# Kernel optimization log

Hardware: AMD Instinct MI355X
Metric: run time of the kernel (lower is better)

The kernel has to match this reference:

```python
import jax, jax.numpy as jnp
import numpy as np

B, N, E, NREG, DIN, F = 16, 20000, 640000, 2000, 128, 32
NEG_SLOPE = 0.2  # PyG GATConv default negative_slope


def setup_inputs() -> dict:
    key = jax.random.key(0)
    ks = jax.random.split(key, 10)
    x = jax.random.normal(ks[0], (B, N, DIN), dtype=jnp.float32)
    edge_src = jnp.sort(jax.random.randint(ks[1], (E,), 0, NREG, dtype=jnp.int64))
    edge_dst = jax.random.randint(ks[2], (E,), 0, N, dtype=jnp.int64)
    edge_attr = jax.random.uniform(ks[3], (B, E, 1), dtype=jnp.float32)
    # GATConv parameters (heads=1, concat=False, edge_dim=1)
    W = jax.random.normal(ks[4], (DIN, F), dtype=jnp.float32) * 0.05   # lin (shared src/dst)
    att_src = jax.random.normal(ks[5], (F,), dtype=jnp.float32) * 0.1
    att_dst = jax.random.normal(ks[6], (F,), dtype=jnp.float32) * 0.1
    lin_edge = jax.random.normal(ks[7], (1, F), dtype=jnp.float32) * 0.1
    att_edge = jax.random.normal(ks[8], (F,), dtype=jnp.float32) * 0.1
    bias = jax.random.normal(ks[9], (F,), dtype=jnp.float32) * 0.01
    return {"x": x, "edge_attr": edge_attr, "W": W, "att_src": att_src,
            "att_dst": att_dst, "lin_edge": lin_edge, "att_edge": att_edge,
            "bias": bias, "edge_src": edge_src, "edge_dst": edge_dst}


def _gat_regulon(x, eattr, W, att_src, att_dst, lin_edge, att_edge, bias,
                 src, dst):
    # x: [N, DIN], eattr: [E, 1]; src/dst: [E] int (src < NREG, sorted)
    h = x @ W                                  # [N, F]
    a_src = h @ att_src                        # [N]
    a_dst = h @ att_dst                        # [N]
    # add_self_loops=True with fill_value='mean' for edge_attr
    loop_attr = jnp.broadcast_to(jnp.mean(eattr, axis=0, keepdims=True), (N, 1))
    eattr_full = jnp.concatenate([eattr, loop_attr], axis=0)         # [E+N, 1]
    sl = jnp.arange(N, dtype=src.dtype)
    src_f = jnp.concatenate([src, sl])                               # [E+N]
    dst_f = jnp.concatenate([dst, sl])                               # [E+N]
    a_edge = (eattr_full @ lin_edge) @ att_edge                      # [E+N]
    alpha = jax.nn.leaky_relu(a_src[src_f] + a_dst[dst_f] + a_edge, NEG_SLOPE)
    # segment softmax over destination nodes (self-loops => no empty segment)
    m = jax.ops.segment_max(alpha, dst_f, num_segments=N)
    ex = jnp.exp(alpha - m[dst_f])
    s = jax.ops.segment_sum(ex, dst_f, num_segments=N)
    coef = ex / s[dst_f]                                             # [E+N]
    rep = jax.ops.segment_sum(coef[:, None] * h[src_f], dst_f, num_segments=N)
    rep = rep + bias                                                 # [N, F]
    # fused regulon pooling: out[i] = rep[i] + sum_{(i->t) in E} rep[t]
    pooled = jax.ops.segment_sum(rep[dst], src, num_segments=NREG)   # [NREG, F]
    return rep[:NREG] + pooled


def reference(x, edge_attr, W, att_src, att_dst, lin_edge, att_edge, bias,
              edge_src, edge_dst):
    fn = jax.vmap(lambda xi, ei: _gat_regulon(xi, ei, W, att_src, att_dst,
                                              lin_edge, att_edge, bias,
                                              edge_src, edge_dst))
    return fn(x, edge_attr)                                          # [B, NREG, F]
```

## Files before the change

### kernel.cpp

```cpp
#include <hip/hip_runtime.h>
#include <math.h>

#define B    16
#define N    20000
#define E    640000
#define NREG 2000
#define DIN  128
#define F    32
#define NEG  0.2f
#define BF   (B * F)
#define NCHUNK 8
#define CS   2500

typedef unsigned int uint;

__device__ inline uint bf16pair(float a, float b) {
    uint ua = __float_as_uint(a); ua = (ua + 0x7fffu + ((ua >> 16) & 1u)) >> 16;
    uint ub = __float_as_uint(b); ub = (ub + 0x7fffu + ((ub >> 16) & 1u)) >> 16;
    return ua | (ub << 16);
}
__device__ inline float bf16lo(uint v) { return __uint_as_float(v << 16); }
__device__ inline float bf16hi(uint v) { return __uint_as_float(v & 0xffff0000u); }

__global__ void k_hist(const int* __restrict__ dst, int* __restrict__ counts) {
    int e = blockIdx.x * blockDim.x + threadIdx.x;
    int stride = gridDim.x * blockDim.x;
    for (; e < E; e += stride)
        atomicAdd(&counts[dst[e]], 1);
}

__global__ void k_roff(const int* __restrict__ esrc, int* __restrict__ roff) {
    int r = blockIdx.x * blockDim.x + threadIdx.x;
    if (r > NREG) return;
    int lo = 0, hi = E;
    while (lo < hi) {
        int mid = (lo + hi) >> 1;
        if (esrc[mid] < r) lo = mid + 1; else hi = mid;
    }
    roff[r] = lo;
}

__global__ void k_scan(const int* __restrict__ in, int* __restrict__ out, int n) {
    __shared__ int sh[1024];
    int t = threadIdx.x;
    int chunk = (n + 1023) / 1024;
    int lo = t * chunk;
    int hi = lo + chunk; if (hi > n) hi = n;
    int local = 0;
    for (int i = lo; i < hi; ++i) local += in[i];
    sh[t] = local;
    __syncthreads();
    for (int d = 1; d < 1024; d <<= 1) {
        int v = (t >= d) ? sh[t - d] : 0;
        __syncthreads();
        sh[t] += v;
        __syncthreads();
    }
    int run = (t == 0) ? 0 : sh[t - 1];
    for (int i = lo; i < hi; ++i) { out[i] = run; run += in[i]; }
    if (t == 1023) out[n] = sh[1023];
}

__global__ void k_scatter(const int* __restrict__ src, const int* __restrict__ dst,
                          const int* __restrict__ off, int* __restrict__ cursor,
                          int* __restrict__ csr_src, int* __restrict__ pos_of_e) {
    int e = blockIdx.x * blockDim.x + threadIdx.x;
    int stride = gridDim.x * blockDim.x;
    for (; e < E; e += stride) {
        int d = dst[e];
        int pos = off[d] + atomicAdd(&cursor[d], 1);
        csr_src[pos] = src[e];
        pos_of_e[e] = pos;
    }
}

__global__ __launch_bounds__(256) void k_bucket(const int* __restrict__ edst,
                                                const int* __restrict__ roff,
                                                int* __restrict__ boff,
                                                int* __restrict__ pe_dst) {
    __shared__ int cnt[NCHUNK], pref[NCHUNK], cur[NCHUNK];
    int r = blockIdx.x;
    int t = threadIdx.x;
    int lo = roff[r], hi = roff[r + 1];
    if (t < NCHUNK) { cnt[t] = 0; cur[t] = 0; }
    __syncthreads();
    for (int e = lo + t; e < hi; e += 256)
        atomicAdd(&cnt[edst[e] / CS], 1);
    __syncthreads();
    if (t == 0) {
        int run = 0;
        #pragma unroll
        for (int c = 0; c < NCHUNK; ++c) { pref[c] = run; run += cnt[c]; }
    }
    __syncthreads();
    if (t < NCHUNK) boff[r * NCHUNK + t] = lo + pref[t];
    if (r == 0 && t == 0) boff[NREG * NCHUNK] = E;
    for (int e = lo + t; e < hi; e += 256) {
        int d = edst[e];
        int c = d / CS;
        int pos = lo + pref[c] + atomicAdd(&cur[c], 1);
        pe_dst[pos] = d;
    }
}

#define MEAN_BLOCKS_PER_B 64
__global__ void k_mean(const float* __restrict__ eattr, float* __restrict__ meanb) {
    int b   = blockIdx.x / MEAN_BLOCKS_PER_B;
    int blk = blockIdx.x % MEAN_BLOCKS_PER_B;
    int per = (E + MEAN_BLOCKS_PER_B - 1) / MEAN_BLOCKS_PER_B;
    int lo = blk * per;
    int hi = lo + per; if (hi > E) hi = E;
    float s = 0.f;
    for (int i = lo + threadIdx.x; i < hi; i += blockDim.x)
        s += eattr[(size_t)b * E + i];
    __shared__ float sh[256];
    sh[threadIdx.x] = s;
    __syncthreads();
    for (int d = 128; d > 0; d >>= 1) {
        if (threadIdx.x < d) sh[threadIdx.x] += sh[threadIdx.x + d];
        __syncthreads();
    }
    if (threadIdx.x == 0) atomicAdd(&meanb[b], sh[0]);
}

__global__ void k_cedge(const float* __restrict__ lin_edge,
                        const float* __restrict__ att_edge, float* __restrict__ c) {
    if (threadIdx.x == 0) {
        float s = 0.f;
        for (int f = 0; f < F; ++f) s += lin_edge[f] * att_edge[f];
        *c = s;
    }
}

__global__ __launch_bounds__(256) void k_edgew(const float* __restrict__ eattr,
                                               const int* __restrict__ esrc,
                                               const int* __restrict__ edst,
                                               const int* __restrict__ pos_of_e,
                                               const float* __restrict__ a_src,
                                               const float* __restrict__ a_dst,
                                               const float* __restrict__ cedge,
                                               float* __restrict__ wbuf) {
    __shared__ float tile[B][257];
    __shared__ int ssrc[256], sdst[256], spos[256];
    int e0 = blockIdx.x * 256;
    int t = threadIdx.x;
    #pragma unroll
    for (int b = 0; b < B; ++b)
        tile[b][t] = eattr[(size_t)b * E + e0 + t];
    ssrc[t] = esrc[e0 + t];
    sdst[t] = edst[e0 + t];
    spos[t] = pos_of_e[e0 + t];
    __syncthreads();
    float c = *cedge;
    #pragma unroll
    for (int p = 0; p < 16; ++p) {
        int idx = p * 256 + t;
        int el = idx >> 4;
        int bb = idx & 15;
        float a = a_src[(size_t)ssrc[el] * B + bb]
                + a_dst[(size_t)sdst[el] * B + bb]
                + tile[bb][el] * c;
        a = a > 0.f ? a : NEG * a;
        wbuf[(size_t)spos[el] * B + bb] = __expf(a);
    }
}

#define XS_LD 260
__global__ __launch_bounds__(256) void k_gemm(const float* __restrict__ x,
                                              const float* __restrict__ W,
                                              const float* __restrict__ att_src,
                                              const float* __restrict__ att_dst,
                                              uint* __restrict__ hu,
                                              float* __restrict__ a_src,
                                              float* __restrict__ a_dst) {
    __shared__ float Ws[DIN * F];
    __shared__ float xs[32 * XS_LD];
    int t = threadIdx.x;
    int row0 = blockIdx.x * 256;
    #pragma unroll
    for (int j = 0; j < 4; ++j) {
        int idx = (t + 256 * j) * 4;
        *(float4*)&Ws[idx] = *(const float4*)&W[idx];
    }
    const int lr = t & 63;
    const int fg = t >> 6;
    float acc[4][8];
    #pragma unroll
    for (int i = 0; i < 4; ++i)
        #pragma unroll
        for (int j = 0; j < 8; ++j) acc[i][j] = 0.f;

    for (int kc = 0; kc < 4; ++kc) {
        __syncthreads();
        #pragma unroll
        for (int j = 0; j < 8; ++j) {
            int p = t + 256 * j;
            int row = p >> 3;
            int kk  = (p & 7) * 4;
            float4 g = *(const float4*)&x[(size_t)(row0 + row) * DIN + kc * 32 + kk];
            xs[(kk + 0) * XS_LD + row] = g.x;
            xs[(kk + 1) * XS_LD + row] = g.y;
            xs[(kk + 2) * XS_LD + row] = g.z;
            xs[(kk + 3) * XS_LD + row] = g.w;
        }
        __syncthreads();
        #pragma unroll
        for (int k = 0; k < 32; ++k) {
            float4 xv = *(float4*)&xs[k * XS_LD + 4 * lr];
            float4 w0 = *(float4*)&Ws[(kc * 32 + k) * F + fg * 8];
            float4 w1 = *(float4*)&Ws[(kc * 32 + k) * F + fg * 8 + 4];
            float xr[4] = {xv.x, xv.y, xv.z, xv.w};
            float wr[8] = {w0.x, w0.y, w0.z, w0.w, w1.x, w1.y, w1.z, w1.w};
            #pragma unroll
            for (int i = 0; i < 4; ++i)
                #pragma unroll
                for (int j = 0; j < 8; ++j)
                    acc[i][j] = fmaf(xr[i], wr[j], acc[i][j]);
        }
    }
    #pragma unroll
    for (int i = 0; i < 4; ++i) {
        int row = row0 + lr * 4 + i;
        int b = row / N;
        int n = row - b * N;
        uint4 o;
        o.x = bf16pair(acc[i][0], acc[i][1]);
        o.y = bf16pair(acc[i][2], acc[i][3]);
        o.z = bf16pair(acc[i][4], acc[i][5]);
        o.w = bf16pair(acc[i][6], acc[i][7]);
        *(uint4*)&hu[(size_t)n * 256 + b * 16 + fg * 4] = o;
    }
    float* red = xs;
    __syncthreads();
    #pragma unroll
    for (int i = 0; i < 4; ++i) {
        float s1 = 0.f, s2 = 0.f;
        #pragma unroll
        for (int j = 0; j < 8; ++j) {
            float as = att_src[fg * 8 + j];
            float ad = att_dst[fg * 8 + j];
            s1 = fmaf(acc[i][j], as, s1);
            s2 = fmaf(acc[i][j], ad, s2);
        }
        red[fg * 256 + lr * 4 + i]        = s1;
        red[1024 + fg * 256 + lr * 4 + i] = s2;
    }
    __syncthreads();
    {
        float s1 = red[t] + red[256 + t] + red[512 + t] + red[768 + t];
        float s2 = red[1024 + t] + red[1280 + t] + red[1536 + t] + red[1792 + t];
        int row = row0 + t;
        int b = row / N;
        int n = row - b * N;
        a_src[(size_t)n * B + b] = s1;
        a_dst[(size_t)n * B + b] = s2;
    }
}

__global__ __launch_bounds__(256) void k_rep(
    const uint* __restrict__ hu, const float* __restrict__ a_src,
    const float* __restrict__ a_dst, const float* __restrict__ wbuf,
    const float* __restrict__ bias, const float* __restrict__ meanb,
    const float* __restrict__ cedge, const int* __restrict__ dst_off,
    const int* __restrict__ csr_src, uint* __restrict__ repu) {
    int i = blockIdx.x;
    int t = threadIdx.x;
    int b  = t >> 4;
    int fp = t & 15;
    float c = *cedge;
    float meanv = meanb[b] * (1.f / (float)E);
    float al = a_src[(size_t)i * B + b] + a_dst[(size_t)i * B + b] + meanv * c;
    al = al > 0.f ? al : NEG * al;
    float s = __expf(al);
    uint hv = hu[(size_t)i * 256 + t];
    float acc0 = s * bf16lo(hv);
    float acc1 = s * bf16hi(hv);
    int lo = dst_off[i], hi = dst_off[i + 1];
    int j = lo;
    for (; j + 4 <= hi; j += 4) {
        int s0 = csr_src[j], s1 = csr_src[j+1], s2 = csr_src[j+2], s3 = csr_src[j+3];
        float w0 = wbuf[(size_t)(j+0) * B + b];
        float w1 = wbuf[(size_t)(j+1) * B + b];
        float w2 = wbuf[(size_t)(j+2) * B + b];
        float w3 = wbuf[(size_t)(j+3) * B + b];
        uint v0 = hu[(size_t)s0 * 256 + t];
        uint v1 = hu[(size_t)s1 * 256 + t];
        uint v2 = hu[(size_t)s2 * 256 + t];
        uint v3 = hu[(size_t)s3 * 256 + t];
        s += w0 + w1 + w2 + w3;
        acc0 = fmaf(w0, bf16lo(v0), acc0);
        acc1 = fmaf(w0, bf16hi(v0), acc1);
        acc0 = fmaf(w1, bf16lo(v1), acc0);
        acc1 = fmaf(w1, bf16hi(v1), acc1);
        acc0 = fmaf(w2, bf16lo(v2), acc0);
        acc1 = fmaf(w2, bf16hi(v2), acc1);
        acc0 = fmaf(w3, bf16lo(v3), acc0);
        acc1 = fmaf(w3, bf16hi(v3), acc1);
    }
    for (; j < hi; ++j) {
        int sj = csr_src[j];
        float wv = wbuf[(size_t)j * B + b];
        uint v = hu[(size_t)sj * 256 + t];
        s += wv;
        acc0 = fmaf(wv, bf16lo(v), acc0);
        acc1 = fmaf(wv, bf16hi(v), acc1);
    }
    float inv = 1.f / s;
    repu[(size_t)i * 256 + t] = bf16pair(acc0 * inv + bias[2 * fp],
                                         acc1 * inv + bias[2 * fp + 1]);
}

__global__ __launch_bounds__(256) void k_pool(const uint* __restrict__ repu,
                                              const int* __restrict__ boff,
                                              const int* __restrict__ pe_dst,
                                              float* __restrict__ partial) {
    int key = blockIdx.x;
    int c = key / NREG;
    int r = key - c * NREG;
    int idx = r * NCHUNK + c;
    int t = threadIdx.x;
    int lo = boff[idx], hi = boff[idx + 1];
    float acc0 = 0.f, acc1 = 0.f;
    int e = lo;
    for (; e + 8 <= hi; e += 8) {
        int d0 = pe_dst[e+0], d1 = pe_dst[e+1], d2 = pe_dst[e+2], d3 = pe_dst[e+3];
        int d4 = pe_dst[e+4], d5 = pe_dst[e+5], d6 = pe_dst[e+6], d7 = pe_dst[e+7];
        uint v0 = repu[(size_t)d0 * 256 + t];
        uint v1 = repu[(size_t)d1 * 256 + t];
        uint v2 = repu[(size_t)d2 * 256 + t];
        uint v3 = repu[(size_t)d3 * 256 + t];
        uint v4 = repu[(size_t)d4 * 256 + t];
        uint v5 = repu[(size_t)d5 * 256 + t];
        uint v6 = repu[(size_t)d6 * 256 + t];
        uint v7 = repu[(size_t)d7 * 256 + t];
        acc0 += (bf16lo(v0) + bf16lo(v1)) + (bf16lo(v2) + bf16lo(v3))
              + (bf16lo(v4) + bf16lo(v5)) + (bf16lo(v6) + bf16lo(v7));
        acc1 += (bf16hi(v0) + bf16hi(v1)) + (bf16hi(v2) + bf16hi(v3))
              + (bf16hi(v4) + bf16hi(v5)) + (bf16hi(v6) + bf16hi(v7));
    }
    for (; e < hi; ++e) {
        int d = pe_dst[e];
        uint v = repu[(size_t)d * 256 + t];
        acc0 += bf16lo(v);
        acc1 += bf16hi(v);
    }
    float2 o = {acc0, acc1};
    *(float2*)&partial[((size_t)r * NCHUNK + c) * BF + 2 * t] = o;
}

__global__ __launch_bounds__(256) void k_combine(const uint* __restrict__ repu,
                                                 const float* __restrict__ partial,
                                                 float* __restrict__ out) {
    int r = blockIdx.x;
    int t = threadIdx.x;
    int b  = t >> 4;
    int fp = t & 15;
    uint v = repu[(size_t)r * 256 + t];
    float s0 = bf16lo(v), s1 = bf16hi(v);
    #pragma unroll
    for (int c = 0; c < NCHUNK; ++c) {
        float2 p = *(const float2*)&partial[((size_t)r * NCHUNK + c) * BF + 2 * t];
        s0 += p.x; s1 += p.y;
    }
    float2 o = {s0, s1};
    *(float2*)&out[(size_t)b * NREG * F + r * F + 2 * fp] = o;
}

extern "C" void kernel_launch(void* const* d_in, const int* in_sizes, int n_in,
                              void* d_out, int out_size, void* d_ws, size_t ws_size,
                              hipStream_t stream) {
    const float* x        = (const float*)d_in[0];
    const float* eattr    = (const float*)d_in[1];
    const float* W        = (const float*)d_in[2];
    const float* att_src  = (const float*)d_in[3];
    const float* att_dst  = (const float*)d_in[4];
    const float* lin_edge = (const float*)d_in[5];
    const float* att_edge = (const float*)d_in[6];
    const float* bias     = (const float*)d_in[7];
    const int*   esrc     = (const int*)d_in[8];
    const int*   edst     = (const int*)d_in[9];
    float* out = (float*)d_out;

    char* ws = (char*)d_ws;
    size_t off = 0;
    auto alloc = [&](size_t bytes) -> void* {
        void* p = ws + off;
        off = (off + bytes + 255) & ~(size_t)255;
        return p;
    };
    uint*  hu    = (uint*)alloc((size_t)N * 256 * 4);
    uint*  repu  = (uint*)alloc((size_t)N * 256 * 4);
    float* wbuf  = (float*)alloc((size_t)E * B * 4);
    float* a_src = (float*)alloc((size_t)N * B * 4);
    float* a_dst = (float*)alloc((size_t)N * B * 4);
    int* dst_off = (int*)alloc((size_t)(N + 1) * 4);
    int* roff    = (int*)alloc((size_t)(NREG + 1) * 4);
    int* csr_src = (int*)alloc((size_t)E * 4);
    int* pos_of_e= (int*)alloc((size_t)E * 4);
    int* pe_dst  = (int*)alloc((size_t)E * 4);
    int* boff    = (int*)alloc((size_t)(NREG * NCHUNK + 1) * 4);
    char* zbase   = ws + off;
    int* counts   = (int*)alloc((size_t)N * 4);
    int* cursor   = (int*)alloc((size_t)N * 4);
    float* meanb  = (float*)alloc((size_t)B * 4);
    float* cedge  = (float*)alloc(4);
    size_t zbytes = (size_t)((ws + off) - zbase);
    float* partial = wbuf;

    hipMemsetAsync(zbase, 0, zbytes, stream);

    k_hist<<<1024, 256, 0, stream>>>(edst, counts);
    k_scan<<<1, 1024, 0, stream>>>(counts, dst_off, N);
    k_roff<<<(NREG + 256) / 256, 256, 0, stream>>>(esrc, roff);
    k_scatter<<<1024, 256, 0, stream>>>(esrc, edst, dst_off, cursor,
                                        csr_src, pos_of_e);
    k_bucket<<<NREG, 256, 0, stream>>>(edst, roff, boff, pe_dst);
    k_mean<<<B * MEAN_BLOCKS_PER_B, 256, 0, stream>>>(eattr, meanb);
    k_cedge<<<1, 64, 0, stream>>>(lin_edge, att_edge, cedge);
    k_gemm<<<(B * N) / 256, 256, 0, stream>>>(x, W, att_src, att_dst,
                                              hu, a_src, a_dst);
    k_edgew<<<E / 256, 256, 0, stream>>>(eattr, esrc, edst, pos_of_e,
                                         a_src, a_dst, cedge, wbuf);
    k_rep<<<N, 256, 0, stream>>>(hu, a_src, a_dst, wbuf, bias, meanb, cedge,
                                 dst_off, csr_src, repu);
    k_pool<<<NREG * NCHUNK, 256, 0, stream>>>(repu, boff, pe_dst, partial);
    k_combine<<<NREG, 256, 0, stream>>>(repu, partial, out);
}
```

Before: 552.5 us.

## Merge preprocessing kernels, fold edge-attr mean into edge-weight pass, unroll gather by 8

Merges the histogram, region-offset search and edge-constant kernels into one launch, and the CSR scatter and per-region bucket kernels into another, using block-index ranges to pick the role. The separate edge-attribute mean kernel is removed; its sum is now computed from the eattr tile already staged in shared memory inside the edge-weight kernel. This removes one full read of edge_attr and several launches. The rep aggregation loop gains an 8-way unrolled gather to put more loads in flight, at the cost of more registers and many more float atomics on meanb.

```diff
diff --git a/kernel.cpp b/kernel.cpp
--- a/kernel.cpp
+++ b/kernel.cpp
@@ -11,6 +11,8 @@
 #define BF   (B * F)
 #define NCHUNK 8
 #define CS   2500
+#define HIST_BLOCKS 1024
+#define SCAT_BLOCKS 1024
 
 typedef unsigned int uint;
 
@@ -22,25 +24,39 @@
 __device__ inline float bf16lo(uint v) { return __uint_as_float(v << 16); }
 __device__ inline float bf16hi(uint v) { return __uint_as_float(v & 0xffff0000u); }
 
-__global__ void k_hist(const int* __restrict__ dst, int* __restrict__ counts) {
-    int e = blockIdx.x * blockDim.x + threadIdx.x;
-    int stride = gridDim.x * blockDim.x;
-    for (; e < E; e += stride)
-        atomicAdd(&counts[dst[e]], 1);
-}
-
-__global__ void k_roff(const int* __restrict__ esrc, int* __restrict__ roff) {
-    int r = blockIdx.x * blockDim.x + threadIdx.x;
-    if (r > NREG) return;
-    int lo = 0, hi = E;
-    while (lo < hi) {
-        int mid = (lo + hi) >> 1;
-        if (esrc[mid] < r) lo = mid + 1; else hi = mid;
-    }
-    roff[r] = lo;
-}
-
-__global__ void k_scan(const int* __restrict__ in, int* __restrict__ out, int n) {
+__global__ __launch_bounds__(256) void k_prep1(const int* __restrict__ esrc,
+                                               const int* __restrict__ edst,
+                                               const float* __restrict__ lin_edge,
+                                               const float* __restrict__ att_edge,
+                                               int* __restrict__ counts,
+                                               int* __restrict__ roff,
+                                               float* __restrict__ cedge) {
+    int blk = blockIdx.x;
+    int t = threadIdx.x;
+    if (blk < HIST_BLOCKS) {
+        int e = blk * 256 + t;
+        for (; e < E; e += HIST_BLOCKS * 256)
+            atomicAdd(&counts[edst[e]], 1);
+    } else if (blk < HIST_BLOCKS + 8) {
+        int r = (blk - HIST_BLOCKS) * 256 + t;
+        if (r > NREG) return;
+        int lo = 0, hi = E;
+        while (lo < hi) {
+            int mid = (lo + hi) >> 1;
+            if (esrc[mid] < r) lo = mid + 1; else hi = mid;
+        }
+        roff[r] = lo;
+    } else {
+        if (t == 0) {
+            float s = 0.f;
+            for (int f = 0; f < F; ++f) s += lin_edge[f] * att_edge[f];
+            *cedge = s;
+        }
+    }
+}
+
+__global__ __launch_bounds__(1024) void k_scan(const int* __restrict__ in,
+                                               int* __restrict__ out, int n) {
     __shared__ int sh[1024];
     int t = threadIdx.x;
     int chunk = (n + 1023) / 1024;
@@ -61,74 +77,48 @@
     if (t == 1023) out[n] = sh[1023];
 }
 
-__global__ void k_scatter(const int* __restrict__ src, const int* __restrict__ dst,
-                          const int* __restrict__ off, int* __restrict__ cursor,
-                          int* __restrict__ csr_src, int* __restrict__ pos_of_e) {
-    int e = blockIdx.x * blockDim.x + threadIdx.x;
-    int stride = gridDim.x * blockDim.x;
-    for (; e < E; e += stride) {
-        int d = dst[e];
-        int pos = off[d] + atomicAdd(&cursor[d], 1);
-        csr_src[pos] = src[e];
-        pos_of_e[e] = pos;
-    }
-}
-
-__global__ __launch_bounds__(256) void k_bucket(const int* __restrict__ edst,
-                                                const int* __restrict__ roff,
-                                                int* __restrict__ boff,
-                                                int* __restrict__ pe_dst) {
+__global__ __launch_bounds__(256) void k_prep2(const int* __restrict__ esrc,
+                                               const int* __restrict__ edst,
+                                               const int* __restrict__ off,
+                                               int* __restrict__ cursor,
+                                               int* __restrict__ csr_src,
+                                               int* __restrict__ pos_of_e,
+                                               const int* __restrict__ roff,
+                                               int* __restrict__ boff,
+                                               int* __restrict__ pe_dst) {
     __shared__ int cnt[NCHUNK], pref[NCHUNK], cur[NCHUNK];
-    int r = blockIdx.x;
-    int t = threadIdx.x;
-    int lo = roff[r], hi = roff[r + 1];
-    if (t < NCHUNK) { cnt[t] = 0; cur[t] = 0; }
-    __syncthreads();
-    for (int e = lo + t; e < hi; e += 256)
-        atomicAdd(&cnt[edst[e] / CS], 1);
-    __syncthreads();
-    if (t == 0) {
-        int run = 0;
-        #pragma unroll
-        for (int c = 0; c < NCHUNK; ++c) { pref[c] = run; run += cnt[c]; }
-    }
-    __syncthreads();
-    if (t < NCHUNK) boff[r * NCHUNK + t] = lo + pref[t];
-    if (r == 0 && t == 0) boff[NREG * NCHUNK] = E;
-    for (int e = lo + t; e < hi; e += 256) {
-        int d = edst[e];
-        int c = d / CS;
-        int pos = lo + pref[c] + atomicAdd(&cur[c], 1);
-        pe_dst[pos] = d;
-    }
-}
-
-#define MEAN_BLOCKS_PER_B 64
-__global__ void k_mean(const float* __restrict__ eattr, float* __restrict__ meanb) {
-    int b   = blockIdx.x / MEAN_BLOCKS_PER_B;
-    int blk = blockIdx.x % MEAN_BLOCKS_PER_B;
-    int per = (E + MEAN_BLOCKS_PER_B - 1) / MEAN_BLOCKS_PER_B;
-    int lo = blk * per;
-    int hi = lo + per; if (hi > E) hi = E;
-    float s = 0.f;
-    for (int i = lo + threadIdx.x; i < hi; i += blockDim.x)
-        s += eattr[(size_t)b * E + i];
-    __shared__ float sh[256];
-    sh[threadIdx.x] = s;
-    __syncthreads();
-    for (int d = 128; d > 0; d >>= 1) {
-        if (threadIdx.x < d) sh[threadIdx.x] += sh[threadIdx.x + d];
-        __syncthreads();
-    }
-    if (threadIdx.x == 0) atomicAdd(&meanb[b], sh[0]);
-}
-
-__global__ void k_cedge(const float* __restrict__ lin_edge,
-                        const float* __restrict__ att_edge, float* __restrict__ c) {
-    if (threadIdx.x == 0) {
-        float s = 0.f;
-        for (int f = 0; f < F; ++f) s += lin_edge[f] * att_edge[f];
-        *c = s;
+    int blk = blockIdx.x;
+    int t = threadIdx.x;
+    if (blk < SCAT_BLOCKS) {
+        int e = blk * 256 + t;
+        for (; e < E; e += SCAT_BLOCKS * 256) {
+            int d = edst[e];
+            int pos = off[d] + atomicAdd(&cursor[d], 1);
+            csr_src[pos] = esrc[e];
+            pos_of_e[e] = pos;
+        }
+    } else {
+        int r = blk - SCAT_BLOCKS;
+        int lo = roff[r], hi = roff[r + 1];
+        if (t < NCHUNK) { cnt[t] = 0; cur[t] = 0; }
+        __syncthreads();
+        for (int e = lo + t; e < hi; e += 256)
+            atomicAdd(&cnt[edst[e] / CS], 1);
+        __syncthreads();
+        if (t == 0) {
+            int run = 0;
+            #pragma unroll
+            for (int c = 0; c < NCHUNK; ++c) { pref[c] = run; run += cnt[c]; }
+        }
+        __syncthreads();
+        if (t < NCHUNK) boff[r * NCHUNK + t] = lo + pref[t];
+        if (r == 0 && t == 0) boff[NREG * NCHUNK] = E;
+        for (int e = lo + t; e < hi; e += 256) {
+            int d = edst[e];
+            int c = d / CS;
+            int pos = lo + pref[c] + atomicAdd(&cur[c], 1);
+            pe_dst[pos] = d;
+        }
     }
 }
 
@@ -139,7 +129,8 @@
                                                const float* __restrict__ a_src,
                                                const float* __restrict__ a_dst,
                                                const float* __restrict__ cedge,
-                                               float* __restrict__ wbuf) {
+                                               float* __restrict__ wbuf,
+                                               float* __restrict__ meanb) {
     __shared__ float tile[B][257];
     __shared__ int ssrc[256], sdst[256], spos[256];
     int e0 = blockIdx.x * 256;
@@ -151,6 +142,15 @@
     sdst[t] = edst[e0 + t];
     spos[t] = pos_of_e[e0 + t];
     __syncthreads();
+    {
+        int bb = t >> 4, fp = t & 15;
+        float ms = 0.f;
+        #pragma unroll
+        for (int q = 0; q < 16; ++q) ms += tile[bb][fp + 16 * q];
+        #pragma unroll
+        for (int d = 8; d > 0; d >>= 1) ms += __shfl_down(ms, d, 16);
+        if (fp == 0) atomicAdd(&meanb[bb], ms);
+    }
     float c = *cedge;
     #pragma unroll
     for (int p = 0; p < 16; ++p) {
@@ -277,6 +277,23 @@
     float acc1 = s * bf16hi(hv);
     int lo = dst_off[i], hi = dst_off[i + 1];
     int j = lo;
+    for (; j + 8 <= hi; j += 8) {
+        int   sv[8];
+        float wv[8];
+        uint  vv[8];
+        #pragma unroll
+        for (int q = 0; q < 8; ++q) sv[q] = csr_src[j + q];
+        #pragma unroll
+        for (int q = 0; q < 8; ++q) wv[q] = wbuf[(size_t)(j + q) * B + b];
+        #pragma unroll
+        for (int q = 0; q < 8; ++q) vv[q] = hu[(size_t)sv[q] * 256 + t];
+        #pragma unroll
+        for (int q = 0; q < 8; ++q) {
+            s += wv[q];
+            acc0 = fmaf(wv[q], bf16lo(vv[q]), acc0);
+            acc1 = fmaf(wv[q], bf16hi(vv[q]), acc1);
+        }
+    }
     for (; j + 4 <= hi; j += 4) {
         int s0 = csr_src[j], s1 = csr_src[j+1], s2 = csr_src[j+2], s3 = csr_src[j+3];
         float w0 = wbuf[(size_t)(j+0) * B + b];
@@ -409,18 +426,16 @@
 
     hipMemsetAsync(zbase, 0, zbytes, stream);
 
-    k_hist<<<1024, 256, 0, stream>>>(edst, counts);
+    k_prep1<<<HIST_BLOCKS + 8 + 1, 256, 0, stream>>>(esrc, edst, lin_edge,
+                                                     att_edge, counts, roff, cedge);
     k_scan<<<1, 1024, 0, stream>>>(counts, dst_off, N);
-    k_roff<<<(NREG + 256) / 256, 256, 0, stream>>>(esrc, roff);
-    k_scatter<<<1024, 256, 0, stream>>>(esrc, edst, dst_off, cursor,
-                                        csr_src, pos_of_e);
-    k_bucket<<<NREG, 256, 0, stream>>>(edst, roff, boff, pe_dst);
-    k_mean<<<B * MEAN_BLOCKS_PER_B, 256, 0, stream>>>(eattr, meanb);
-    k_cedge<<<1, 64, 0, stream>>>(lin_edge, att_edge, cedge);
+    k_prep2<<<SCAT_BLOCKS + NREG, 256, 0, stream>>>(esrc, edst, dst_off, cursor,
+                                                    csr_src, pos_of_e,
+                                                    roff, boff, pe_dst);
     k_gemm<<<(B * N) / 256, 256, 0, stream>>>(x, W, att_src, att_dst,
                                               hu, a_src, a_dst);
     k_edgew<<<E / 256, 256, 0, stream>>>(eattr, esrc, edst, pos_of_e,
-                                         a_src, a_dst, cedge, wbuf);
+                                         a_src, a_dst, cedge, wbuf, meanb);
     k_rep<<<N, 256, 0, stream>>>(hu, a_src, a_dst, wbuf, bias, meanb, cedge,
                                  dst_off, csr_src, repu);
     k_pool<<<NREG * NCHUNK, 256, 0, stream>>>(repu, boff, pe_dst, partial);
```

Result: slower. 613.7 us (+11.1%).
